# Kernel optimization log

Measured on AMD Instinct MI355X. Metric: run time of the kernel, lower is better.

The kernel has to match this reference:

```python
import jax, jax.numpy as jnp
import numpy as np

B, N, D = 2, 2048, 1024
H = 16
DH = D // H

def setup_inputs() -> dict:
    key = jax.random.key(0)
    ks = jax.random.split(key, 9)
    s = 1.0 / np.sqrt(D)
    return {
        "x": jax.random.normal(ks[0], (B, N, D), dtype=jnp.float32),
        "Wq": jax.random.uniform(ks[1], (D, D), jnp.float32, -s, s),
        "bq": jax.random.uniform(ks[2], (D,), jnp.float32, -s, s),
        "Wk": jax.random.uniform(ks[3], (D, D), jnp.float32, -s, s),
        "bk": jax.random.uniform(ks[4], (D,), jnp.float32, -s, s),
        "Wv": jax.random.uniform(ks[5], (D, D), jnp.float32, -s, s),
        "bv": jax.random.uniform(ks[6], (D,), jnp.float32, -s, s),
        "Wo": jax.random.uniform(ks[7], (D, D), jnp.float32, -s, s),
        "bo": jax.random.uniform(ks[8], (D,), jnp.float32, -s, s),
    }

def reference(x, Wq, bq, Wk, bk, Wv, bv, Wo, bo):
    # torch Linear: y = x @ W.T + b
    scale = 1.0 / np.sqrt(DH)
    q = (x @ Wq.T + bq).reshape(B, N, H, DH).transpose(0, 2, 1, 3)  # [B,H,N,DH]
    k = (x @ Wk.T + bk).reshape(B, N, H, DH).transpose(0, 2, 1, 3)
    v = (x @ Wv.T + bv).reshape(B, N, H, DH).transpose(0, 2, 1, 3)
    scores = jnp.einsum('bhnd,bhmd->bhnm', q, k) * scale  # [B,H,N,N]
    attn = jax.nn.softmax(scores, axis=-1)
    out = jnp.einsum('bhnm,bhmd->bhnd', attn, v)  # [B,H,N,DH]
    out = out.transpose(0, 2, 1, 3).reshape(B, N, D)
    return out @ Wo.T + bo
```

## Files before the change

### kernel.cpp

```cpp
#include <hip/hip_runtime.h>
#include <hip/hip_bf16.h>

#define B_  2
#define N_  2048
#define D_  1024
#define H_  16
#define DH_ 64
#define BN_ (B_*N_)

typedef __attribute__((ext_vector_type(8))) short short8;
typedef __attribute__((ext_vector_type(4))) float f32x4;
typedef __attribute__((ext_vector_type(16))) float f32x16;
typedef __attribute__((ext_vector_type(4))) unsigned int uint4v;

typedef __attribute__((address_space(3))) unsigned int lds_u32_t;
typedef const __attribute__((address_space(1))) unsigned int glb_u32_t;

__device__ __forceinline__ void async_load16(const unsigned short* g, unsigned short* l) {
    __builtin_amdgcn_global_load_lds((glb_u32_t*)g, (lds_u32_t*)l, 16, 0, 0);
}

__device__ __forceinline__ unsigned short f2bf(float f) {
    __hip_bfloat16 h = __float2bfloat16(f);
    return *reinterpret_cast<unsigned short*>(&h);
}

__device__ __forceinline__ unsigned int pkbf(float a, float b) {
    unsigned int ua = __float_as_uint(a) + 0x8000u;
    unsigned int ub = __float_as_uint(b) + 0x8000u;
    return __builtin_amdgcn_perm(ub, ua, 0x07060302);
}

#if __has_builtin(__builtin_amdgcn_exp2f)
#define EXP2(x) __builtin_amdgcn_exp2f(x)
#else
#define EXP2(x) exp2f(x)
#endif

#define QSCL 0.1803368801111204f

__global__ __launch_bounds__(256) void cast_kernel(
    const float* __restrict__ x,  const float* __restrict__ wq,
    const float* __restrict__ wk, const float* __restrict__ wv,
    const float* __restrict__ wo,
    unsigned short* __restrict__ xb,  unsigned short* __restrict__ wqb,
    unsigned short* __restrict__ wkb, unsigned short* __restrict__ wvb,
    unsigned short* __restrict__ wob)
{
    const size_t NX = (size_t)BN_ * D_;
    const size_t NW = (size_t)D_ * D_;
    size_t i = ((size_t)blockIdx.x * 256 + threadIdx.x) * 4;
    const float* src; unsigned short* dst; size_t off;
    if (i < NX) { src = x; dst = xb; off = i; }
    else {
        size_t j = (i - NX) >> 20;
        off = (i - NX) & (NW - 1);
        src = (j == 0) ? wq : (j == 1) ? wk : (j == 2) ? wv : wo;
        dst = (j == 0) ? wqb : (j == 1) ? wkb : (j == 2) ? wvb : wob;
    }
    float4 v = *(const float4*)(src + off);
    ushort4 o;
    o.x = f2bf(v.x); o.y = f2bf(v.y); o.z = f2bf(v.z); o.w = f2bf(v.w);
    *(ushort4*)(dst + off) = o;
}

template<int OUT_MODE>
__device__ __forceinline__ void gemm_body(
    unsigned short* __restrict__ As, unsigned short* __restrict__ Bs,
    const unsigned short* __restrict__ A, const unsigned short* __restrict__ W,
    const float* __restrict__ bias, void* __restrict__ Cout, int bx, int by)
{
    constexpr int K = D_;
    const int tid  = threadIdx.x;
    const int lane = tid & 63;
    const int wave = tid >> 6;
    const int wm = wave & 1, wn = wave >> 1;
    const int l15 = lane & 15, quad = lane >> 4;

    f32x4 acc[4][4] = {};
    const int row0 = by * 128, col0 = bx * 128;

    const int srow = lane >> 3;
    const int scb  = lane & 7;

    for (int k0 = 0; k0 < K; k0 += 64) {
        __syncthreads();
#pragma unroll
        for (int cc = 0; cc < 4; ++cc) {
            int c  = wave * 4 + cc;
            int lr = c * 8 + srow;
            int gcol = k0 + ((scb ^ (lr & 7)) * 8);
            async_load16(A + (size_t)(row0 + lr) * K + gcol, As + c * 512);
            async_load16(W + (size_t)(col0 + lr) * K + gcol, Bs + c * 512);
        }
        __syncthreads();

#pragma unroll
        for (int kf = 0; kf < 2; ++kf) {
            const int swz = ((kf * 4 + quad) ^ (l15 & 7)) * 8;
            short8 af[4], bf[4];
#pragma unroll
            for (int mi = 0; mi < 4; mi++)
                af[mi] = *(const short8*)(&As[(wm * 64 + mi * 16 + l15) * 64 + swz]);
#pragma unroll
            for (int ni = 0; ni < 4; ni++)
                bf[ni] = *(const short8*)(&Bs[(wn * 64 + ni * 16 + l15) * 64 + swz]);
#pragma unroll
            for (int mi = 0; mi < 4; mi++)
#pragma unroll
                for (int ni = 0; ni < 4; ni++)
                    acc[mi][ni] = __builtin_amdgcn_mfma_f32_16x16x32_bf16(
                        af[mi], bf[ni], acc[mi][ni], 0, 0, 0);
        }
    }

    if (OUT_MODE == 2) {
        __syncthreads();
#pragma unroll
        for (int ni = 0; ni < 4; ni++) {
            int c = wn * 64 + ni * 16 + l15;
            float bv = bias[col0 + c];
#pragma unroll
            for (int mi = 0; mi < 4; mi++) {
                int r = wm * 64 + mi * 16 + quad * 4;
                ushort4 pk;
                pk.x = f2bf(acc[mi][ni][0] + bv);
                pk.y = f2bf(acc[mi][ni][1] + bv);
                pk.z = f2bf(acc[mi][ni][2] + bv);
                pk.w = f2bf(acc[mi][ni][3] + bv);
                unsigned short* base = (c < 64) ? (As + c * 128) : (Bs + (c - 64) * 128);
                *(ushort4*)(base + (r ^ ((c & 7) << 3))) = pk;
            }
        }
        __syncthreads();
#pragma unroll
        for (int itx = 0; itx < 8; ++itx) {
            int item = itx * 256 + tid;
            int c  = item >> 4;
            int rb = item & 15;
            const unsigned short* base = (c < 64) ? (As + c * 128) : (Bs + (c - 64) * 128);
            uint4v v = *(const uint4v*)(base + ((rb ^ (c & 7)) * 8));
            *(uint4v*)((unsigned short*)Cout + (size_t)(col0 + c) * BN_ + row0 + rb * 8) = v;
        }
        return;
    }

#pragma unroll
    for (int ni = 0; ni < 4; ni++) {
        int col = col0 + wn * 64 + ni * 16 + l15;
        float bv = bias[col];
#pragma unroll
        for (int mi = 0; mi < 4; mi++) {
            int row = row0 + wm * 64 + mi * 16 + quad * 4;
#pragma unroll
            for (int r = 0; r < 4; r++) {
                float v = acc[mi][ni][r] + bv;
                if (OUT_MODE == 3) v *= QSCL;
                if (OUT_MODE == 0)
                    ((float*)Cout)[(size_t)(row + r) * D_ + col] = v;
                else
                    ((unsigned short*)Cout)[(size_t)(row + r) * D_ + col] = f2bf(v);
            }
        }
    }
}

__device__ __forceinline__ void xcd_swz(int& bx, int& by) {
    int w = blockIdx.y * 8 + blockIdx.x;
    int s = (w & 7) * 32 + (w >> 3);
    bx = s & 7; by = s >> 3;
}

__global__ __launch_bounds__(256) void qkv_gemm(
    const unsigned short* __restrict__ xb,
    const unsigned short* __restrict__ wqb, const unsigned short* __restrict__ wkb,
    const unsigned short* __restrict__ wvb,
    const float* __restrict__ bq, const float* __restrict__ bk, const float* __restrict__ bv,
    unsigned short* __restrict__ q, unsigned short* __restrict__ k, unsigned short* __restrict__ vt)
{
    __shared__ __align__(16) unsigned short As[128 * 64];
    __shared__ __align__(16) unsigned short Bs[128 * 64];
    int bx, by; xcd_swz(bx, by);
    if (blockIdx.z == 0)
        gemm_body<3>(As, Bs, xb, wqb, bq, q,  bx, by);
    else if (blockIdx.z == 1)
        gemm_body<1>(As, Bs, xb, wkb, bk, k,  bx, by);
    else
        gemm_body<2>(As, Bs, xb, wvb, bv, vt, bx, by);
}

__global__ __launch_bounds__(256) void out_gemm(
    const unsigned short* __restrict__ attn, const unsigned short* __restrict__ wob,
    const float* __restrict__ bo, float* __restrict__ out)
{
    __shared__ __align__(16) unsigned short As[128 * 64];
    __shared__ __align__(16) unsigned short Bs[128 * 64];
    int bx, by; xcd_swz(bx, by);
    gemm_body<0>(As, Bs, attn, wob, bo, out, bx, by);
}

__global__ __launch_bounds__(256) void attn_kernel(
    const unsigned short* __restrict__ q, const unsigned short* __restrict__ k,
    const unsigned short* __restrict__ vt, unsigned short* __restrict__ o)
{
    __shared__ __align__(16) unsigned short Ks[2][64 * 64];
    __shared__ __align__(16) unsigned short Vs[2][64 * 64];

    const int tid = threadIdx.x;
    const int lane = tid & 63, wave = tid >> 6;
    const int l31 = lane & 31, kq = lane >> 5;
    const int bh = blockIdx.x;
    const int qt = blockIdx.y;
    const int b = bh >> 4, h = bh & 15;

    const unsigned short* qb = q  + (size_t)b * N_ * D_ + h * DH_;
    const unsigned short* kb = k  + (size_t)b * N_ * D_ + h * DH_;
    const unsigned short* vb = vt + (size_t)h * DH_ * BN_ + (size_t)b * N_;

    const int qrow0 = qt * 128 + wave * 32;

    short8 qf[4];
#pragma unroll
    for (int s = 0; s < 4; s++)
        qf[s] = *(const short8*)(qb + (size_t)(qrow0 + l31) * D_ + s * 16 + kq * 8);

    f32x16 oacc[2] = {};
    float lsum = 0.f;

    const int srow = lane >> 3, scb = lane & 7;

    auto stage = [&](int bi, int kv0) {
#pragma unroll
        for (int cc = 0; cc < 2; ++cc) {
            int c  = wave * 2 + cc;
            int lr = c * 8 + srow;
            int swz8 = (scb ^ (lr & 7)) * 8;
            async_load16(kb + (size_t)(kv0 + lr) * D_ + swz8, (unsigned short*)Ks[bi] + c * 512);
            async_load16(vb + (size_t)lr * BN_ + kv0 + swz8,  (unsigned short*)Vs[bi] + c * 512);
        }
    };

    stage(0, 0);

    const int NIT = N_ / 64;
    for (int it = 0; it < NIT; ++it) {
        const int cur = it & 1;
        __syncthreads();
        if (it + 1 < NIT) stage(cur ^ 1, (it + 1) * 64);

        const unsigned short* Kc = Ks[cur];
        const unsigned short* Vc = Vs[cur];

        f32x16 st[2] = {};
#pragma unroll
        for (int s = 0; s < 4; s++) {
#pragma unroll
            for (int mb = 0; mb < 2; mb++) {
                short8 kfr = *(const short8*)((const char*)Kc +
                    (mb * 32 + l31) * 128 + (((2 * s + kq) ^ (l31 & 7)) * 16));
                st[mb] = __builtin_amdgcn_mfma_f32_32x32x16_bf16(
                    kfr, qf[s], st[mb], 0, 0, 0);
            }
        }

#pragma unroll
        for (int mb = 0; mb < 2; mb++) {
            unsigned int pk[8];
#pragma unroll
            for (int g = 0; g < 4; g++) {
                float p0 = EXP2(st[mb][g * 4 + 0]);
                float p1 = EXP2(st[mb][g * 4 + 1]);
                float p2 = EXP2(st[mb][g * 4 + 2]);
                float p3 = EXP2(st[mb][g * 4 + 3]);
                lsum += (p0 + p1) + (p2 + p3);
                pk[2 * g + 0] = pkbf(p0, p1);
                pk[2 * g + 1] = pkbf(p2, p3);
            }
#pragma unroll
            for (int s = 0; s < 2; s++) {
                uint4v fu;
                fu[0] = pk[4 * s + 0]; fu[1] = pk[4 * s + 1];
                fu[2] = pk[4 * s + 2]; fu[3] = pk[4 * s + 3];
                short8 pf = __builtin_bit_cast(short8, fu);
                const int blkA = 4 * mb + 2 * s;
#pragma unroll
                for (int nb = 0; nb < 2; nb++) {
                    const char* vrow = (const char*)Vc + (nb * 32 + l31) * 128;
                    uint2 vlo = *(const uint2*)(vrow + ((blkA       ^ (l31 & 7)) * 16) + kq * 8);
                    uint2 vhi = *(const uint2*)(vrow + (((blkA + 1) ^ (l31 & 7)) * 16) + kq * 8);
                    uint4v vu; vu[0] = vlo.x; vu[1] = vlo.y; vu[2] = vhi.x; vu[3] = vhi.y;
                    short8 vf = __builtin_bit_cast(short8, vu);
                    oacc[nb] = __builtin_amdgcn_mfma_f32_32x32x16_bf16(
                        pf, vf, oacc[nb], 0, 0, 0);
                }
            }
        }
    }

    lsum += __shfl_xor(lsum, 32);
    __syncthreads();
    float* Lt = (float*)&Ks[0][0] + wave * 32;
    if (kq == 0) Lt[l31] = lsum;
    asm volatile("s_waitcnt lgkmcnt(0)" ::: "memory");

#pragma unroll
    for (int g = 0; g < 4; g++)
#pragma unroll
        for (int rr = 0; rr < 4; rr++) {
            int reg = g * 4 + rr;
            float inv = 1.f / Lt[rr + 8 * g + 4 * kq];
            int row = qrow0 + rr + 8 * g + 4 * kq;
            size_t base = ((size_t)b * N_ + row) * D_ + h * DH_;
#pragma unroll
            for (int nb = 0; nb < 2; nb++)
                o[base + nb * 32 + l31] = f2bf(oacc[nb][reg] * inv);
        }
}

extern "C" void kernel_launch(void* const* d_in, const int* in_sizes, int n_in,
                              void* d_out, int out_size, void* d_ws, size_t ws_size,
                              hipStream_t stream)
{
    const float* x  = (const float*)d_in[0];
    const float* Wq = (const float*)d_in[1];
    const float* bq = (const float*)d_in[2];
    const float* Wk = (const float*)d_in[3];
    const float* bk = (const float*)d_in[4];
    const float* Wv = (const float*)d_in[5];
    const float* bv = (const float*)d_in[6];
    const float* Wo = (const float*)d_in[7];
    const float* bo = (const float*)d_in[8];
    float* out = (float*)d_out;

    char* ws = (char*)d_ws;
    unsigned short* xb  = (unsigned short*)(ws + 0);
    unsigned short* wqb = (unsigned short*)(ws + 8388608);
    unsigned short* wkb = (unsigned short*)(ws + 10485760);
    unsigned short* wvb = (unsigned short*)(ws + 12582912);
    unsigned short* wob = (unsigned short*)(ws + 14680064);
    unsigned short* qd  = (unsigned short*)(ws + 16777216);
    unsigned short* kd  = (unsigned short*)(ws + 25165824);
    unsigned short* vtd = (unsigned short*)(ws + 33554432);
    unsigned short* ad  = (unsigned short*)(ws + 41943040);

    cast_kernel<<<8192, 256, 0, stream>>>(x, Wq, Wk, Wv, Wo, xb, wqb, wkb, wvb, wob);
    qkv_gemm<<<dim3(8, 32, 3), 256, 0, stream>>>(xb, wqb, wkb, wvb, bq, bk, bv, qd, kd, vtd);
    attn_kernel<<<dim3(32, 16), 256, 0, stream>>>(qd, kd, vtd, ad);
    out_gemm<<<dim3(8, 32), 256, 0, stream>>>(ad, wob, bo, out);
}
```

Measured before the change: 204.4 us.

## Double-buffer GEMM LDS tiles and raise wave priority around attention MFMAs

The shared GEMM body now keeps two LDS buffers and prefetches the next K-slice with async global-to-LDS loads while the current one is consumed by MFMAs. This removes the second barrier per iteration and lets memory latency overlap compute. LDS per block doubles to 64 KB, which may lower occupancy. The attention kernel also wraps its MFMA sections in s_setprio so that waves issuing matrix ops get scheduling preference over waves doing softmax math.

```diff
diff --git a/kernel.cpp b/kernel.cpp
--- a/kernel.cpp
+++ b/kernel.cpp
@@ -71,6 +71,7 @@
     const float* __restrict__ bias, void* __restrict__ Cout, int bx, int by)
 {
     constexpr int K = D_;
+    constexpr int NT = K / 64;
     const int tid  = threadIdx.x;
     const int lane = tid & 63;
     const int wave = tid >> 6;
@@ -83,17 +84,28 @@
     const int srow = lane >> 3;
     const int scb  = lane & 7;
 
-    for (int k0 = 0; k0 < K; k0 += 64) {
-        __syncthreads();
+    auto stage = [&](int bi, int k0) {
+        unsigned short* Ad = As + bi * 8192;
+        unsigned short* Bd = Bs + bi * 8192;
 #pragma unroll
         for (int cc = 0; cc < 4; ++cc) {
             int c  = wave * 4 + cc;
             int lr = c * 8 + srow;
             int gcol = k0 + ((scb ^ (lr & 7)) * 8);
-            async_load16(A + (size_t)(row0 + lr) * K + gcol, As + c * 512);
-            async_load16(W + (size_t)(col0 + lr) * K + gcol, Bs + c * 512);
-        }
+            async_load16(A + (size_t)(row0 + lr) * K + gcol, Ad + c * 512);
+            async_load16(W + (size_t)(col0 + lr) * K + gcol, Bd + c * 512);
+        }
+    };
+
+    stage(0, 0);
+
+    for (int t = 0; t < NT; ++t) {
+        const int cur = t & 1;
         __syncthreads();
+        if (t + 1 < NT) stage(cur ^ 1, (t + 1) * 64);
+
+        const unsigned short* Ac = As + cur * 8192;
+        const unsigned short* Bc = Bs + cur * 8192;
 
 #pragma unroll
         for (int kf = 0; kf < 2; ++kf) {
@@ -101,10 +113,10 @@
             short8 af[4], bf[4];
 #pragma unroll
             for (int mi = 0; mi < 4; mi++)
-                af[mi] = *(const short8*)(&As[(wm * 64 + mi * 16 + l15) * 64 + swz]);
+                af[mi] = *(const short8*)(&Ac[(wm * 64 + mi * 16 + l15) * 64 + swz]);
 #pragma unroll
             for (int ni = 0; ni < 4; ni++)
-                bf[ni] = *(const short8*)(&Bs[(wn * 64 + ni * 16 + l15) * 64 + swz]);
+                bf[ni] = *(const short8*)(&Bc[(wn * 64 + ni * 16 + l15) * 64 + swz]);
 #pragma unroll
             for (int mi = 0; mi < 4; mi++)
 #pragma unroll
@@ -128,8 +140,7 @@
                 pk.y = f2bf(acc[mi][ni][1] + bv);
                 pk.z = f2bf(acc[mi][ni][2] + bv);
                 pk.w = f2bf(acc[mi][ni][3] + bv);
-                unsigned short* base = (c < 64) ? (As + c * 128) : (Bs + (c - 64) * 128);
-                *(ushort4*)(base + (r ^ ((c & 7) << 3))) = pk;
+                *(ushort4*)(As + c * 128 + (r ^ ((c & 7) << 3))) = pk;
             }
         }
         __syncthreads();
@@ -138,8 +149,7 @@
             int item = itx * 256 + tid;
             int c  = item >> 4;
             int rb = item & 15;
-            const unsigned short* base = (c < 64) ? (As + c * 128) : (Bs + (c - 64) * 128);
-            uint4v v = *(const uint4v*)(base + ((rb ^ (c & 7)) * 8));
+            uint4v v = *(const uint4v*)(As + c * 128 + ((rb ^ (c & 7)) * 8));
             *(uint4v*)((unsigned short*)Cout + (size_t)(col0 + c) * BN_ + row0 + rb * 8) = v;
         }
         return;
@@ -178,8 +188,8 @@
     const float* __restrict__ bq, const float* __restrict__ bk, const float* __restrict__ bv,
     unsigned short* __restrict__ q, unsigned short* __restrict__ k, unsigned short* __restrict__ vt)
 {
-    __shared__ __align__(16) unsigned short As[128 * 64];
-    __shared__ __align__(16) unsigned short Bs[128 * 64];
+    __shared__ __align__(16) unsigned short As[2 * 128 * 64];
+    __shared__ __align__(16) unsigned short Bs[2 * 128 * 64];
     int bx, by; xcd_swz(bx, by);
     if (blockIdx.z == 0)
         gemm_body<3>(As, Bs, xb, wqb, bq, q,  bx, by);
@@ -193,8 +203,8 @@
     const unsigned short* __restrict__ attn, const unsigned short* __restrict__ wob,
     const float* __restrict__ bo, float* __restrict__ out)
 {
-    __shared__ __align__(16) unsigned short As[128 * 64];
-    __shared__ __align__(16) unsigned short Bs[128 * 64];
+    __shared__ __align__(16) unsigned short As[2 * 128 * 64];
+    __shared__ __align__(16) unsigned short Bs[2 * 128 * 64];
     int bx, by; xcd_swz(bx, by);
     gemm_body<0>(As, Bs, attn, wob, bo, out, bx, by);
 }
@@ -252,6 +262,7 @@
         const unsigned short* Vc = Vs[cur];
 
         f32x16 st[2] = {};
+        __builtin_amdgcn_s_setprio(1);
 #pragma unroll
         for (int s = 0; s < 4; s++) {
 #pragma unroll
@@ -262,6 +273,7 @@
                     kfr, qf[s], st[mb], 0, 0, 0);
             }
         }
+        __builtin_amdgcn_s_setprio(0);
 
 #pragma unroll
         for (int mb = 0; mb < 2; mb++) {
@@ -276,6 +288,7 @@
                 pk[2 * g + 0] = pkbf(p0, p1);
                 pk[2 * g + 1] = pkbf(p2, p3);
             }
+            __builtin_amdgcn_s_setprio(1);
 #pragma unroll
             for (int s = 0; s < 2; s++) {
                 uint4v fu;
@@ -294,6 +307,7 @@
                         pf, vf, oacc[nb], 0, 0, 0);
                 }
             }
+            __builtin_amdgcn_s_setprio(0);
         }
     }
 
```

After: 203.2 us. About the same (-0.6%).

## Shrink GEMM tiles to 64x128 for more blocks and add MFMA priority hints

Applied to the files above, without the earlier changes.

Both projection GEMMs now use 64x128 output tiles instead of 128x128. Each wave covers all 64 rows and 32 columns, the grid doubles in the row dimension, and the XCD swizzle and launch bounds are updated to match. The aim is to give the 256 CUs more blocks, which helps the out-projection most since it had only 256 blocks, and to let more blocks reside per CU, at the cost of lower arithmetic intensity per tile. The attention kernel also raises wave priority around its MFMA sections so matrix work can interleave better with the softmax exp phase.

```diff
diff --git a/kernel.cpp b/kernel.cpp
--- a/kernel.cpp
+++ b/kernel.cpp
@@ -74,23 +74,28 @@
     const int tid  = threadIdx.x;
     const int lane = tid & 63;
     const int wave = tid >> 6;
-    const int wm = wave & 1, wn = wave >> 1;
     const int l15 = lane & 15, quad = lane >> 4;
 
-    f32x4 acc[4][4] = {};
-    const int row0 = by * 128, col0 = bx * 128;
+    f32x4 acc[4][2] = {};
+    const int row0 = by * 64, col0 = bx * 128;
 
     const int srow = lane >> 3;
     const int scb  = lane & 7;
 
     for (int k0 = 0; k0 < K; k0 += 64) {
         __syncthreads();
+#pragma unroll
+        for (int cc = 0; cc < 2; ++cc) {
+            int c  = wave * 2 + cc;
+            int lr = c * 8 + srow;
+            int gcol = k0 + ((scb ^ (lr & 7)) * 8);
+            async_load16(A + (size_t)(row0 + lr) * K + gcol, As + c * 512);
+        }
 #pragma unroll
         for (int cc = 0; cc < 4; ++cc) {
             int c  = wave * 4 + cc;
             int lr = c * 8 + srow;
             int gcol = k0 + ((scb ^ (lr & 7)) * 8);
-            async_load16(A + (size_t)(row0 + lr) * K + gcol, As + c * 512);
             async_load16(W + (size_t)(col0 + lr) * K + gcol, Bs + c * 512);
         }
         __syncthreads();
@@ -98,17 +103,17 @@
 #pragma unroll
         for (int kf = 0; kf < 2; ++kf) {
             const int swz = ((kf * 4 + quad) ^ (l15 & 7)) * 8;
-            short8 af[4], bf[4];
+            short8 af[4], bf[2];
 #pragma unroll
             for (int mi = 0; mi < 4; mi++)
-                af[mi] = *(const short8*)(&As[(wm * 64 + mi * 16 + l15) * 64 + swz]);
-#pragma unroll
-            for (int ni = 0; ni < 4; ni++)
-                bf[ni] = *(const short8*)(&Bs[(wn * 64 + ni * 16 + l15) * 64 + swz]);
+                af[mi] = *(const short8*)(&As[(mi * 16 + l15) * 64 + swz]);
+#pragma unroll
+            for (int ni = 0; ni < 2; ni++)
+                bf[ni] = *(const short8*)(&Bs[(wave * 32 + ni * 16 + l15) * 64 + swz]);
 #pragma unroll
             for (int mi = 0; mi < 4; mi++)
 #pragma unroll
-                for (int ni = 0; ni < 4; ni++)
+                for (int ni = 0; ni < 2; ni++)
                     acc[mi][ni] = __builtin_amdgcn_mfma_f32_16x16x32_bf16(
                         af[mi], bf[ni], acc[mi][ni], 0, 0, 0);
         }
@@ -117,41 +122,39 @@
     if (OUT_MODE == 2) {
         __syncthreads();
 #pragma unroll
-        for (int ni = 0; ni < 4; ni++) {
-            int c = wn * 64 + ni * 16 + l15;
+        for (int ni = 0; ni < 2; ni++) {
+            int c = wave * 32 + ni * 16 + l15;
             float bv = bias[col0 + c];
 #pragma unroll
             for (int mi = 0; mi < 4; mi++) {
-                int r = wm * 64 + mi * 16 + quad * 4;
+                int r = mi * 16 + quad * 4;
                 ushort4 pk;
                 pk.x = f2bf(acc[mi][ni][0] + bv);
                 pk.y = f2bf(acc[mi][ni][1] + bv);
                 pk.z = f2bf(acc[mi][ni][2] + bv);
                 pk.w = f2bf(acc[mi][ni][3] + bv);
-                unsigned short* base = (c < 64) ? (As + c * 128) : (Bs + (c - 64) * 128);
-                *(ushort4*)(base + (r ^ ((c & 7) << 3))) = pk;
-            }
-        }
-        __syncthreads();
-#pragma unroll
-        for (int itx = 0; itx < 8; ++itx) {
+                *(ushort4*)(Bs + c * 64 + (r ^ ((c & 7) << 3))) = pk;
+            }
+        }
+        __syncthreads();
+#pragma unroll
+        for (int itx = 0; itx < 4; ++itx) {
             int item = itx * 256 + tid;
-            int c  = item >> 4;
-            int rb = item & 15;
-            const unsigned short* base = (c < 64) ? (As + c * 128) : (Bs + (c - 64) * 128);
-            uint4v v = *(const uint4v*)(base + ((rb ^ (c & 7)) * 8));
+            int c  = item >> 3;
+            int rb = item & 7;
+            uint4v v = *(const uint4v*)(Bs + c * 64 + ((rb ^ (c & 7)) * 8));
             *(uint4v*)((unsigned short*)Cout + (size_t)(col0 + c) * BN_ + row0 + rb * 8) = v;
         }
         return;
     }
 
 #pragma unroll
-    for (int ni = 0; ni < 4; ni++) {
-        int col = col0 + wn * 64 + ni * 16 + l15;
+    for (int ni = 0; ni < 2; ni++) {
+        int col = col0 + wave * 32 + ni * 16 + l15;
         float bv = bias[col];
 #pragma unroll
         for (int mi = 0; mi < 4; mi++) {
-            int row = row0 + wm * 64 + mi * 16 + quad * 4;
+            int row = row0 + mi * 16 + quad * 4;
 #pragma unroll
             for (int r = 0; r < 4; r++) {
                 float v = acc[mi][ni][r] + bv;
@@ -167,18 +170,18 @@
 
 __device__ __forceinline__ void xcd_swz(int& bx, int& by) {
     int w = blockIdx.y * 8 + blockIdx.x;
-    int s = (w & 7) * 32 + (w >> 3);
+    int s = (w & 7) * 64 + (w >> 3);
     bx = s & 7; by = s >> 3;
 }
 
-__global__ __launch_bounds__(256) void qkv_gemm(
+__global__ __launch_bounds__(256, 5) void qkv_gemm(
     const unsigned short* __restrict__ xb,
     const unsigned short* __restrict__ wqb, const unsigned short* __restrict__ wkb,
     const unsigned short* __restrict__ wvb,
     const float* __restrict__ bq, const float* __restrict__ bk, const float* __restrict__ bv,
     unsigned short* __restrict__ q, unsigned short* __restrict__ k, unsigned short* __restrict__ vt)
 {
-    __shared__ __align__(16) unsigned short As[128 * 64];
+    __shared__ __align__(16) unsigned short As[64 * 64];
     __shared__ __align__(16) unsigned short Bs[128 * 64];
     int bx, by; xcd_swz(bx, by);
     if (blockIdx.z == 0)
@@ -189,11 +192,11 @@
         gemm_body<2>(As, Bs, xb, wvb, bv, vt, bx, by);
 }
 
-__global__ __launch_bounds__(256) void out_gemm(
+__global__ __launch_bounds__(256, 5) void out_gemm(
     const unsigned short* __restrict__ attn, const unsigned short* __restrict__ wob,
     const float* __restrict__ bo, float* __restrict__ out)
 {
-    __shared__ __align__(16) unsigned short As[128 * 64];
+    __shared__ __align__(16) unsigned short As[64 * 64];
     __shared__ __align__(16) unsigned short Bs[128 * 64];
     int bx, by; xcd_swz(bx, by);
     gemm_body<0>(As, Bs, attn, wob, bo, out, bx, by);
@@ -252,6 +255,7 @@
         const unsigned short* Vc = Vs[cur];
 
         f32x16 st[2] = {};
+        __builtin_amdgcn_s_setprio(1);
 #pragma unroll
         for (int s = 0; s < 4; s++) {
 #pragma unroll
@@ -262,6 +266,7 @@
                     kfr, qf[s], st[mb], 0, 0, 0);
             }
         }
+        __builtin_amdgcn_s_setprio(0);
 
 #pragma unroll
         for (int mb = 0; mb < 2; mb++) {
@@ -276,6 +281,7 @@
                 pk[2 * g + 0] = pkbf(p0, p1);
                 pk[2 * g + 1] = pkbf(p2, p3);
             }
+            __builtin_amdgcn_s_setprio(1);
 #pragma unroll
             for (int s = 0; s < 2; s++) {
                 uint4v fu;
@@ -294,6 +300,7 @@
                         pf, vf, oacc[nb], 0, 0, 0);
                 }
             }
+            __builtin_amdgcn_s_setprio(0);
         }
     }
 
@@ -344,7 +351,7 @@
     unsigned short* ad  = (unsigned short*)(ws + 41943040);
 
     cast_kernel<<<8192, 256, 0, stream>>>(x, Wq, Wk, Wv, Wo, xb, wqb, wkb, wvb, wob);
-    qkv_gemm<<<dim3(8, 32, 3), 256, 0, stream>>>(xb, wqb, wkb, wvb, bq, bk, bv, qd, kd, vtd);
+    qkv_gemm<<<dim3(8, 64, 3), 256, 0, stream>>>(xb, wqb, wkb, wvb, bq, bk, bv, qd, kd, vtd);
     attn_kernel<<<dim3(32, 16), 256, 0, stream>>>(qd, kd, vtd, ad);
-    out_gemm<<<dim3(8, 32), 256, 0, stream>>>(ad, wob, bo, out);
-}
+    out_gemm<<<dim3(8, 64), 256, 0, stream>>>(ad, wob, bo, out);
+}
```

Result: faster. 196.5 us (-3.9%).
